# Performance work log

Measured on AMD Instinct MI355X. Metric: run time of the kernel, lower is better.

Reference implementation:

```python
import jax, jax.numpy as jnp
import numpy as np

B, H, V, T = 32768, 1024, 9, 20
EOS = 8

def setup_inputs() -> dict:
    key = jax.random.key(0)
    ks = jax.random.split(key, 10)
    s_fc = 1.0 / np.sqrt(784)
    s_ih = 1.0 / np.sqrt(V)
    s_hh = 1.0 / np.sqrt(H)
    u = jax.random.uniform(ks[9], (T, B, V), jnp.float32, 1e-10, 1.0)
    return {
        "x": jax.random.normal(ks[0], (B, 784), jnp.float32),
        "tau": jnp.float32(1.0),
        "fc_w": jax.random.normal(ks[1], (H, 784), jnp.float32) * s_fc,
        "w_ih": jax.random.normal(ks[2], (3 * H, V), jnp.float32) * s_ih,
        "w_hh": jax.random.normal(ks[3], (3 * H, H), jnp.float32) * s_hh,
        "b_ih": jax.random.normal(ks[4], (3 * H,), jnp.float32) * s_hh,
        "b_hh": jax.random.normal(ks[5], (3 * H,), jnp.float32) * s_hh,
        "proj_w": jax.random.normal(ks[6], (V, H), jnp.float32) * s_hh,
        "proj_b": jax.random.normal(ks[7], (V,), jnp.float32) * s_hh,
        # standard Gumbel(0,1) noise, precomputed for all T steps
        "gumbel": -jnp.log(-jnp.log(u)),
    }


def reference(x, tau, fc_w, w_ih, w_hh, b_ih, b_hh, proj_w, proj_b, gumbel):
    # context = gelu(fc(x)); dropout is identity (eval mode)
    h0 = jax.nn.gelu(x @ fc_w.T, approximate=False)  # [B, H]
    b = x.shape[0]
    tok0 = jnp.zeros((b, V), x.dtype).at[:, 0].set(1.0)  # BOS one-hot

    def step(carry, g):
        h, tok, finished, lengths, t = carry
        gi = tok @ w_ih.T + b_ih            # [B, 3H]
        gh = h @ w_hh.T + b_hh              # [B, 3H]
        i_r, i_z, i_n = jnp.split(gi, 3, axis=-1)
        h_r, h_z, h_n = jnp.split(gh, 3, axis=-1)
        r = jax.nn.sigmoid(i_r + h_r)
        z = jax.nn.sigmoid(i_z + h_z)
        n = jnp.tanh(i_n + r * h_n)
        h_new = (1.0 - z) * n + z * h
        logits = h_new @ proj_w.T + proj_b  # [B, V]
        y_soft = jax.nn.softmax((logits + g) / tau, axis=-1)
        idx = jnp.argmax(y_soft, axis=-1)
        y_hard = jax.nn.one_hot(idx, V, dtype=y_soft.dtype)
        y = y_hard + y_soft - jax.lax.stop_gradient(y_soft)  # straight-through
        newly = (idx == EOS) & (~finished)
        lengths = jnp.where(newly, t + 1, lengths)
        finished = finished | newly
        return (h_new, y, finished, lengths, t + 1), y

    carry0 = (h0, tok0,
              jnp.zeros((b,), jnp.bool_),
              jnp.full((b,), T, jnp.int32),
              jnp.int32(0))
    (_, _, _, lengths, _), toks = jax.lax.scan(step, carry0, gumbel)
    message = jnp.transpose(toks, (1, 0, 2))  # [B, T, V]
    return message, lengths
```

## Files before the change

### kernel.cpp

```cpp
#include <hip/hip_runtime.h>
#include <math.h>

#define Bsz 32768
#define Hd  1024
#define Vn  9
#define Tn  20
#define EOSv 8
#define KFC 784

typedef float f4 __attribute__((ext_vector_type(4)));
typedef float f32x16 __attribute__((ext_vector_type(16)));
typedef _Float16 h8 __attribute__((ext_vector_type(8)));
typedef unsigned short us4 __attribute__((ext_vector_type(4)));
typedef unsigned short us8v __attribute__((ext_vector_type(8)));

__device__ __forceinline__ unsigned short f16_rne(float x) {
    _Float16 h = (_Float16)x;
    return __builtin_bit_cast(unsigned short, h);
}
__device__ __forceinline__ float f16_val(unsigned short u) {
    return (float)__builtin_bit_cast(_Float16, u);
}
__device__ __forceinline__ void split2h(float x, unsigned short& p0, unsigned short& p1) {
    p0 = f16_rne(x);
    float r = x - f16_val(p0);
    p1 = f16_rne(r);
}

__device__ __forceinline__ void gload16(const void* g, void* l) {
    __builtin_amdgcn_global_load_lds(
        (const __attribute__((address_space(1))) unsigned int*)g,
        (__attribute__((address_space(3))) unsigned int*)l, 16, 0, 0);
}

#define V_WAIT(N) asm volatile("s_waitcnt vmcnt(" #N ")" ::: "memory")
#define BARRIER   asm volatile("s_barrier" ::: "memory")

__global__ __launch_bounds__(256) void k_init(int* __restrict__ st,
                                              float* __restrict__ lenf) {
    int i = blockIdx.x * 256 + threadIdx.x;
    if (i < Bsz) { st[i] = 0; lenf[i] = (float)Tn; }
}

__global__ __launch_bounds__(256) void k_prep(const float* __restrict__ wih,
                                              const float* __restrict__ bih,
                                              float* __restrict__ giTab) {
    int i = blockIdx.x * 256 + threadIdx.x;
    int tk = i / 3072, n = i - tk * 3072;
    giTab[i] = wih[(size_t)n * Vn + tk] + bih[n];
}

__global__ __launch_bounds__(256) void k_prepB(const float* __restrict__ whh,
                                               unsigned short* __restrict__ wp) {
    int g = blockIdx.x * 256 + threadIdx.x;
    int lane = g & 63, u = g >> 6;
    int p = u & 1, kc = (u >> 1) & 63, ct = u >> 7;
    int col = ct * 32 + (lane & 31);
    int k = kc * 16 + (lane >> 5) * 8;
    const float* src = whh + (size_t)col * Hd + k;
    unsigned short v[8];
    #pragma unroll
    for (int i = 0; i < 8; ++i) {
        unsigned short s0, s1; split2h(src[i], s0, s1);
        v[i] = (p == 0) ? s0 : s1;
    }
    unsigned short* dst = wp + (size_t)u * 512 + lane * 8;
    us4 w0; w0[0]=v[0]; w0[1]=v[1]; w0[2]=v[2]; w0[3]=v[3];
    us4 w1; w1[0]=v[4]; w1[1]=v[5]; w1[2]=v[6]; w1[3]=v[7];
    *(us4*)dst = w0;
    *(us4*)(dst + 4) = w1;
}

__global__ __launch_bounds__(256) void k_fcP(const float* __restrict__ x,
                                             const float* __restrict__ fcw,
                                             float* __restrict__ h0,
                                             unsigned short* __restrict__ ap) {
    __shared__ float As[16][68];
    __shared__ float Ws[16][68];
    const int tid = threadIdx.x;
    const int tx = tid & 15, ty = tid >> 4;
    const int m0 = blockIdx.x * 64, n0 = blockIdx.y * 64;
    const int lrow = tid >> 2, lkc = (tid & 3) << 2;
    float acc[4][4] = {};
    for (int k0 = 0; k0 < KFC; k0 += 16) {
        f4 a = *(const f4*)(x   + (size_t)(m0 + lrow) * KFC + k0 + lkc);
        f4 w = *(const f4*)(fcw + (size_t)(n0 + lrow) * KFC + k0 + lkc);
        #pragma unroll
        for (int q = 0; q < 4; ++q) { As[lkc + q][lrow] = a[q]; Ws[lkc + q][lrow] = w[q]; }
        __syncthreads();
        #pragma unroll
        for (int kk = 0; kk < 16; ++kk) {
            f4 av = *(const f4*)&As[kk][ty * 4];
            f4 wv = *(const f4*)&Ws[kk][tx * 4];
            #pragma unroll
            for (int i = 0; i < 4; ++i)
                #pragma unroll
                for (int j = 0; j < 4; ++j)
                    acc[i][j] = fmaf(av[i], wv[j], acc[i][j]);
        }
        __syncthreads();
    }
    #pragma unroll
    for (int i = 0; i < 4; ++i) {
        const int row = m0 + ty * 4 + i;
        const int cb = n0 + tx * 4;
        f4 hv;
        us4 q0, q1;
        #pragma unroll
        for (int j = 0; j < 4; ++j) {
            float v = acc[i][j];
            float gl = 0.5f * v * (1.0f + erff(v * 0.70710678118654752f));
            hv[j] = gl;
            unsigned short s0, s1; split2h(gl, s0, s1);
            q0[j] = s0; q1[j] = s1;
        }
        *(f4*)&h0[(size_t)row * Hd + cb] = hv;
        const size_t ub = ((size_t)(row >> 5) * 64 + (cb >> 4)) * 2;
        const int slot = (row & 31) + ((cb >> 3) & 1) * 32;
        const int eo = (tx & 1) * 4;
        *(us4*)&ap[(ub + 0) * 512 + slot * 8 + eo] = q0;
        *(us4*)&ap[(ub + 1) * 512 + slot * 8 + eo] = q1;
    }
}

__global__ __launch_bounds__(512, 2) void k_step(
        const unsigned short* __restrict__ ap, float* __restrict__ h,
        const unsigned short* __restrict__ wp, const float* __restrict__ bhh,
        const float* __restrict__ giTab, const int* __restrict__ st) {
    __shared__ unsigned short Sm[3][28 * 512];
    const int tid = threadIdx.x;
    const int lane = tid & 63, wid = tid >> 6;
    const int wm = wid >> 1, wn = wid & 1;
    const int l31 = lane & 31, lh = lane >> 5;

    const int w = blockIdx.x;
    const int cg = (w & 7) * 2 + ((w >> 3) & 1);
    const int rb = w >> 4;
    const int m_blk = rb * 256;
    const int c0 = cg * 64;

    f32x16 acc[2][3];
    #pragma unroll
    for (int mt = 0; mt < 2; ++mt)
        #pragma unroll
        for (int g = 0; g < 3; ++g)
            #pragma unroll
            for (int e = 0; e < 16; ++e) acc[mt][g][e] = 0.0f;

    auto stage = [&](int s, int bi) {
        if (wid < 4) {
            #pragma unroll
            for (int j = 0; j < 4; ++j) {
                const int u = wid * 4 + j;
                const int rg = rb * 8 + (u >> 1), p = u & 1;
                const unsigned short* src = ap + ((size_t)(rg * 64 + s) * 2 + p) * 512 + lane * 8;
                gload16(src, &Sm[bi][u * 512]);
            }
        } else {
            #pragma unroll
            for (int j = 0; j < 3; ++j) {
                const int b = (wid - 4) * 3 + j;
                const int wnl = b / 6, rem = b - wnl * 6;
                const int g = rem >> 1, p = rem & 1;
                const int ct = g * 32 + cg * 2 + wnl;
                const unsigned short* src = wp + ((size_t)(ct * 64 + s) * 2 + p) * 512 + lane * 8;
                gload16(src, &Sm[bi][(16 + b) * 512]);
            }
        }
    };
    auto compute = [&](int bi) {
        h8 af[2][2], bf[3][2];
        #pragma unroll
        for (int mt = 0; mt < 2; ++mt)
            #pragma unroll
            for (int p = 0; p < 2; ++p)
                af[mt][p] = *(const h8*)&Sm[bi][(((wm * 2 + mt) * 2 + p)) * 512 + lane * 8];
        #pragma unroll
        for (int g = 0; g < 3; ++g)
            #pragma unroll
            for (int p = 0; p < 2; ++p)
                bf[g][p] = *(const h8*)&Sm[bi][(16 + wn * 6 + g * 2 + p) * 512 + lane * 8];
        #pragma unroll
        for (int ps = 0; ps < 3; ++ps)
            #pragma unroll
            for (int g = 0; g < 3; ++g)
                #pragma unroll
                for (int mt = 0; mt < 2; ++mt) {
                    h8 a = (ps == 1) ? af[mt][1] : af[mt][0];
                    h8 b = (ps == 0) ? bf[g][1] : bf[g][0];
                    acc[mt][g] = __builtin_amdgcn_mfma_f32_32x32x16_f16(a, b, acc[mt][g], 0, 0, 0);
                }
    };

    stage(0, 0);
    stage(1, 1);
    if (wid < 4) { V_WAIT(4); } else { V_WAIT(3); }
    BARRIER;

    for (int s = 0; s < 64; ++s) {
        const int bi = s % 3;
        if (s < 62) stage(s + 2, (s + 2) % 3);
        compute(bi);
        if (s < 63) {
            if (s < 62) { if (wid < 4) { V_WAIT(4); } else { V_WAIT(3); } }
            else        { V_WAIT(0); }
            BARRIER;
        }
    }

    const int col = c0 + wn * 32 + l31;
    const float bhr = bhh[col], bhz = bhh[Hd + col], bhn = bhh[2 * Hd + col];
    #pragma unroll
    for (int mt = 0; mt < 2; ++mt) {
        #pragma unroll
        for (int reg = 0; reg < 16; ++reg) {
            const int row = m_blk + wm * 64 + mt * 32 + 4 * lh + (reg & 3) + 8 * (reg >> 2);
            const int tk = st[row] & 15;
            const float* gi = giTab + tk * 3072;
            float rr = 1.0f / (1.0f + expf(-(gi[col] + acc[mt][0][reg] + bhr)));
            float zz = 1.0f / (1.0f + expf(-(gi[Hd + col] + acc[mt][1][reg] + bhz)));
            float nn = tanhf(gi[2 * Hd + col] + rr * (acc[mt][2][reg] + bhn));
            const size_t off = (size_t)row * Hd + col;
            float hold = h[off];
            h[off] = (1.0f - zz) * nn + zz * hold;
        }
    }
}

__global__ __launch_bounds__(256) void k_projP(const float* __restrict__ hnew,
        unsigned short* __restrict__ ap,
        const float* __restrict__ pw, const float* __restrict__ pb,
        const float* __restrict__ gum, const float* __restrict__ tau,
        float* __restrict__ msg, float* __restrict__ lenf,
        int* __restrict__ st, int t) {
    const int lane = threadIdx.x & 63;
    const int wv = threadIdx.x >> 6;
    const int b = blockIdx.x * 4 + wv;
    const float* hr = hnew + (size_t)b * Hd;
    float s[Vn] = {};
    float vals[16];
    #pragma unroll
    for (int c0 = 0; c0 < 16; c0 += 4) {
        f4 hv = *(const f4*)(hr + lane * 16 + c0);
        #pragma unroll
        for (int q = 0; q < 4; ++q) vals[c0 + q] = hv[q];
        #pragma unroll
        for (int v = 0; v < Vn; ++v) {
            f4 pv = *(const f4*)(pw + (size_t)v * Hd + lane * 16 + c0);
            #pragma unroll
            for (int q = 0; q < 4; ++q) s[v] = fmaf(hv[q], pv[q], s[v]);
        }
    }
    us8v o0[2], o1[2];
    #pragma unroll
    for (int hh = 0; hh < 2; ++hh)
        #pragma unroll
        for (int e = 0; e < 8; ++e) {
            unsigned short q0, q1;
            split2h(vals[hh * 8 + e], q0, q1);
            o0[hh][e] = q0; o1[hh][e] = q1;
        }
    const size_t ub = ((size_t)(b >> 5) * 64 + lane) * 2;
    const int sl = (b & 31) * 8;
    *(us8v*)&ap[(ub + 0) * 512 + sl]       = o0[0];
    *(us8v*)&ap[(ub + 0) * 512 + sl + 256] = o0[1];
    *(us8v*)&ap[(ub + 1) * 512 + sl]       = o1[0];
    *(us8v*)&ap[(ub + 1) * 512 + sl + 256] = o1[1];
    #pragma unroll
    for (int v = 0; v < Vn; ++v)
        #pragma unroll
        for (int off = 32; off > 0; off >>= 1)
            s[v] += __shfl_xor(s[v], off, 64);
    if (lane == 0) {
        const float tv = tau[0];
        float zv[Vn];
        #pragma unroll
        for (int v = 0; v < Vn; ++v)
            zv[v] = (s[v] + pb[v] + gum[(size_t)b * Vn + v]) / tv;
        int idx = 0; float m = zv[0];
        #pragma unroll
        for (int v = 1; v < Vn; ++v)
            if (zv[v] > m) { m = zv[v]; idx = v; }
        float* orow = msg + ((size_t)b * Tn + t) * Vn;
        #pragma unroll
        for (int v = 0; v < Vn; ++v) orow[v] = (v == idx) ? 1.0f : 0.0f;
        const int old = st[b];
        const int fn = old >> 4;
        st[b] = idx | (((fn != 0) || (idx == EOSv)) ? 16 : 0);
        if (idx == EOSv && fn == 0) lenf[b] = (float)(t + 1);
    }
}

extern "C" void kernel_launch(void* const* d_in, const int* in_sizes, int n_in,
                              void* d_out, int out_size, void* d_ws, size_t ws_size,
                              hipStream_t stream) {
    const float* x   = (const float*)d_in[0];
    const float* tau = (const float*)d_in[1];
    const float* fcw = (const float*)d_in[2];
    const float* wih = (const float*)d_in[3];
    const float* whh = (const float*)d_in[4];
    const float* bih = (const float*)d_in[5];
    const float* bhh = (const float*)d_in[6];
    const float* pw  = (const float*)d_in[7];
    const float* pb  = (const float*)d_in[8];
    const float* gum = (const float*)d_in[9];

    float* msg  = (float*)d_out;
    float* lenf = msg + (size_t)Bsz * Tn * Vn;

    char* ws = (char*)d_ws;
    float*          h     = (float*)ws;
    unsigned short* apb   = (unsigned short*)(ws + 134217728ull);
    unsigned short* wpb   = (unsigned short*)(ws + 268435456ull);
    float*          giTab = (float*)(ws + 281018368ull);
    int*            st    = (int*)  (ws + 281128960ull);

    k_init<<<Bsz / 256, 256, 0, stream>>>(st, lenf);
    k_prep<<<108, 256, 0, stream>>>(wih, bih, giTab);
    k_prepB<<<3072, 256, 0, stream>>>(whh, wpb);
    k_fcP<<<dim3(Bsz / 64, Hd / 64), 256, 0, stream>>>(x, fcw, h, apb);
    for (int t = 0; t < Tn; ++t) {
        k_step<<<2048, 512, 0, stream>>>(apb, h, wpb, bhh, giTab, st);
        k_projP<<<Bsz / 4, 256, 0, stream>>>(h, apb, pw, pb,
                                             gum + (size_t)t * Bsz * Vn,
                                             tau, msg, lenf, st, t);
    }
}
```

Baseline: 17.93 ms.

## Double-buffer LDS fragment reads in registers and prefetch one more stage

Splits the per-stage compute into an LDS-read phase and an MFMA phase. Fragments for the next stage are loaded into a second register set while the current stage's 18 MFMAs run. The prologue now stages three global-to-LDS tiles ahead instead of two, and the MFMA block is wrapped in s_setprio to favour matrix issue. The goal is to hide LDS latency and global-load latency behind the matrix math, at the cost of more VGPRs for the duplicated fragments and extra lgkmcnt waits and barriers.

Result: no change. 17.96 ms (+0.2%).

```diff
diff --git a/kernel.cpp b/kernel.cpp
--- a/kernel.cpp
+++ b/kernel.cpp
@@ -34,6 +34,7 @@
 }
 
 #define V_WAIT(N) asm volatile("s_waitcnt vmcnt(" #N ")" ::: "memory")
+#define L_WAIT0   asm volatile("s_waitcnt lgkmcnt(0)" ::: "memory")
 #define BARRIER   asm volatile("s_barrier" ::: "memory")
 
 __global__ __launch_bounds__(256) void k_init(int* __restrict__ st,
@@ -168,8 +169,7 @@
             }
         }
     };
-    auto compute = [&](int bi) {
-        h8 af[2][2], bf[3][2];
+    auto ldsread = [&](int bi, h8 (&af)[2][2], h8 (&bf)[3][2]) {
         #pragma unroll
         for (int mt = 0; mt < 2; ++mt)
             #pragma unroll
@@ -180,6 +180,9 @@
             #pragma unroll
             for (int p = 0; p < 2; ++p)
                 bf[g][p] = *(const h8*)&Sm[bi][(16 + wn * 6 + g * 2 + p) * 512 + lane * 8];
+    };
+    auto mfma18 = [&](h8 (&af)[2][2], h8 (&bf)[3][2]) {
+        __builtin_amdgcn_s_setprio(1);
         #pragma unroll
         for (int ps = 0; ps < 3; ++ps)
             #pragma unroll
@@ -190,21 +193,41 @@
                     h8 b = (ps == 0) ? bf[g][1] : bf[g][0];
                     acc[mt][g] = __builtin_amdgcn_mfma_f32_32x32x16_f16(a, b, acc[mt][g], 0, 0, 0);
                 }
+        __builtin_amdgcn_s_setprio(0);
     };
+
+    h8 afA[2][2], bfA[3][2], afB[2][2], bfB[3][2];
 
     stage(0, 0);
     stage(1, 1);
+    stage(2, 2);
     if (wid < 4) { V_WAIT(4); } else { V_WAIT(3); }
     BARRIER;
-
-    for (int s = 0; s < 64; ++s) {
-        const int bi = s % 3;
-        if (s < 62) stage(s + 2, (s + 2) % 3);
-        compute(bi);
-        if (s < 63) {
-            if (s < 62) { if (wid < 4) { V_WAIT(4); } else { V_WAIT(3); } }
+    ldsread(0, afA, bfA);
+    L_WAIT0;
+    BARRIER;
+
+    for (int h2 = 0; h2 < 32; ++h2) {
+        const int h = h2 * 2;
+        {
+            if (h + 3 < 64) stage(h + 3, (h + 3) % 3);
+            ldsread((h + 1) % 3, afB, bfB);
+            mfma18(afA, bfA);
+            L_WAIT0;
+            if (h < 60) { if (wid < 4) { V_WAIT(4); } else { V_WAIT(3); } }
             else        { V_WAIT(0); }
             BARRIER;
+        }
+        {
+            if (h + 4 < 64) stage(h + 4, (h + 4) % 3);
+            if (h + 2 < 64) ldsread((h + 2) % 3, afA, bfA);
+            mfma18(afB, bfB);
+            if (h + 2 < 64) {
+                L_WAIT0;
+                if (h + 1 < 60) { if (wid < 4) { V_WAIT(4); } else { V_WAIT(3); } }
+                else            { V_WAIT(0); }
+                BARRIER;
+            }
         }
     }
 
```
